# Performance work log

Measured on AMD Instinct MI355X. Metric: run time of the kernel, lower is better.

The kernel has to match this reference:

```python
import jax, jax.numpy as jnp
import numpy as np
import math

BS, N, D_MODEL, H = 8, 1024, 512, 8
D_K = D_MODEL // H


def setup_inputs() -> dict:
    key = jax.random.key(0)
    ks = jax.random.split(key, 12)
    s = 1.0 / math.sqrt(D_MODEL)
    inp = {
        "query": jax.random.normal(ks[0], (BS, N, D_MODEL), jnp.float32),
        "key": jax.random.normal(ks[1], (BS, N, D_MODEL), jnp.float32),
        "value": jax.random.normal(ks[2], (BS, N, D_MODEL), jnp.float32),
        "wc_matrix": jax.random.normal(ks[3], (BS, N, N), jnp.float32),
        "Wq": jax.random.normal(ks[4], (D_MODEL, D_MODEL), jnp.float32) * s,
        "bq": jnp.zeros((D_MODEL,), jnp.float32),
        "Wk": jax.random.normal(ks[5], (D_MODEL, D_MODEL), jnp.float32) * s,
        "bk": jnp.zeros((D_MODEL,), jnp.float32),
        "Wv": jax.random.normal(ks[6], (D_MODEL, D_MODEL), jnp.float32) * s,
        "bv": jnp.zeros((D_MODEL,), jnp.float32),
        "Wo": jax.random.normal(ks[7], (D_MODEL, D_MODEL), jnp.float32) * s,
        "bo": jnp.zeros((D_MODEL,), jnp.float32),
    }
    return inp


def _split_heads(x):
    # (bs, N, d_model) -> (bs, h, N, d_k)
    b, n, _ = x.shape
    return x.reshape(b, n, H, D_K).transpose(0, 2, 1, 3)


def reference(query, key, value, wc_matrix, Wq, bq, Wk, bk, Wv, bv, Wo, bo):
    # Linear projections (torch Linear: x @ W.T + b), split into heads
    q = _split_heads(query @ Wq.T + bq)
    k = _split_heads(key @ Wk.T + bk)
    v = _split_heads(value @ Wv.T + bv)

    # scores: (bs, h, N, N)
    scores = jnp.einsum("bhnd,bhmd->bhnm", q, k) / jnp.sqrt(jnp.float32(D_K))
    # WC modulation: scores * softmax(wc)[:, None] + scores  (softmax_wc=True, residual=True)
    wc_sm = jax.nn.softmax(wc_matrix, axis=-1)[:, None]  # (bs, 1, N, N)
    scores = scores * wc_sm + scores
    p_attn = jax.nn.softmax(scores, axis=-1)  # dropout is identity in eval

    a = jnp.einsum("bhnm,bhmd->bhnd", p_attn, v)
    a = a.transpose(0, 2, 1, 3).reshape(query.shape[0], -1, D_MODEL)
    return a @ Wo.T + bo
```

## Files before the change

### kernel.cpp

```cpp
#include <hip/hip_runtime.h>
#include <math.h>


#define BS 8
#define SEQ 1024
#define DM 512
#define NH 8
#define DK 64
#define ROWS (BS * SEQ)

typedef __bf16 bf16_t;
typedef bf16_t bf16x8 __attribute__((ext_vector_type(8)));
typedef bf16_t bf16x4 __attribute__((ext_vector_type(4)));
typedef float f32x4 __attribute__((ext_vector_type(4)));

__device__ inline f32x4 mfma32(bf16x8 a, bf16x8 b, f32x4 c) {
  return __builtin_amdgcn_mfma_f32_16x16x32_bf16(a, b, c, 0, 0, 0);
}

__device__ inline void gload_lds16(const bf16_t* g, bf16_t* l) {
  __builtin_amdgcn_global_load_lds(
      (const __attribute__((address_space(1))) void*)g,
      (__attribute__((address_space(3))) void*)l, 16, 0, 0);
}

__global__ __launch_bounds__(256) void cvt_kernel(
    const float* q, const float* k, const float* v,
    const float* wq, const float* wk, const float* wv, const float* wo,
    bf16_t* xq, bf16_t* xk, bf16_t* xv,
    bf16_t* wqb, bf16_t* wkb, bf16_t* wvb, bf16_t* wob) {
  const float* srcs[7] = {q, k, v, wq, wk, wv, wo};
  bf16_t* dsts[7] = {xq, xk, xv, wqb, wkb, wvb, wob};
  int b = blockIdx.x;
  int seg, boff;
  if (b < 1536) { seg = b >> 9; boff = b & 511; }
  else { seg = 3 + ((b - 1536) >> 5); boff = (b - 1536) & 31; }
  const float* src = srcs[seg] + (size_t)boff * 8192;
  bf16_t* dst = dsts[seg] + (size_t)boff * 8192;
  int t = threadIdx.x;
#pragma unroll
  for (int f = 0; f < 8; ++f) {
    int idx = (f * 256 + t) * 4;
    float4 x = *(const float4*)(src + idx);
    bf16x4 o;
    o[0] = (bf16_t)x.x; o[1] = (bf16_t)x.y; o[2] = (bf16_t)x.z; o[3] = (bf16_t)x.w;
    *(bf16x4*)(dst + idx) = o;
  }
}

__global__ __launch_bounds__(256) void wc_softmax_kernel(const float* __restrict__ wc,
                                                         bf16_t* __restrict__ G) {
  int row = blockIdx.x;
  const float* x = wc + (size_t)row * SEQ;
  bf16_t* y = G + (size_t)row * SEQ;
  int t = threadIdx.x;
  float4 v = *(const float4*)(x + t * 4);
  float m = fmaxf(fmaxf(v.x, v.y), fmaxf(v.z, v.w));
#pragma unroll
  for (int off = 32; off > 0; off >>= 1) m = fmaxf(m, __shfl_xor(m, off, 64));
  __shared__ float sm[4], ss[4];
  int w = t >> 6;
  if ((t & 63) == 0) sm[w] = m;
  __syncthreads();
  m = fmaxf(fmaxf(sm[0], sm[1]), fmaxf(sm[2], sm[3]));
  float4 e;
  e.x = __expf(v.x - m); e.y = __expf(v.y - m);
  e.z = __expf(v.z - m); e.w = __expf(v.w - m);
  float s = e.x + e.y + e.z + e.w;
#pragma unroll
  for (int off = 32; off > 0; off >>= 1) s += __shfl_xor(s, off, 64);
  if ((t & 63) == 0) ss[w] = s;
  __syncthreads();
  s = ss[0] + ss[1] + ss[2] + ss[3];
  float inv = 1.0f / s;
  const float SC = 0.18033688011112042f;
  bf16x4 g;
  g[0] = (bf16_t)((1.0f + e.x * inv) * SC);
  g[1] = (bf16_t)((1.0f + e.y * inv) * SC);
  g[2] = (bf16_t)((1.0f + e.z * inv) * SC);
  g[3] = (bf16_t)((1.0f + e.w * inv) * SC);
  *(bf16x4*)(y + t * 4) = g;
}

template <int BM, bool OUTF32>
__device__ inline void gemm_core(const bf16_t* X, const bf16_t* W,
                                 const float* bias, void* Cv,
                                 int mblk, int nblk) {
  __shared__ bf16_t As[2][BM * 32];
  __shared__ bf16_t Bs[2][128 * 32];
  int t = threadIdx.x, lane = t & 63, w = t >> 6;
  int quad = lane >> 4, l15 = lane & 15;
  constexpr int MT = BM / 32;
  int m0w = (w & 1) * (BM / 2), n0w = (w >> 1) * 64;
  int mbase = mblk * BM, nbase = nblk * 128;
  int lr = lane >> 2, l4 = lane & 3;
  f32x4 acc[MT][4] = {};

#pragma unroll
  for (int f = 0; f < BM / 64; ++f) {
    int i = f * 4 + w;
    gload_lds16(X + (size_t)(mbase + i * 16 + lr) * DM + l4 * 8, &As[0][i * 512]);
  }
#pragma unroll
  for (int f = 0; f < 2; ++f) {
    int i = f * 4 + w;
    gload_lds16(W + (size_t)(nbase + i * 16 + lr) * DM + l4 * 8, &Bs[0][i * 512]);
  }

  for (int it = 0; it < 16; ++it) {
    __syncthreads();
    int cb = it & 1;
    if (it + 1 < 16) {
      int kb = (it + 1) * 32, nb = (it + 1) & 1;
#pragma unroll
      for (int f = 0; f < BM / 64; ++f) {
        int i = f * 4 + w;
        gload_lds16(X + (size_t)(mbase + i * 16 + lr) * DM + kb + l4 * 8, &As[nb][i * 512]);
      }
#pragma unroll
      for (int f = 0; f < 2; ++f) {
        int i = f * 4 + w;
        gload_lds16(W + (size_t)(nbase + i * 16 + lr) * DM + kb + l4 * 8, &Bs[nb][i * 512]);
      }
    }
    bf16x8 af[MT], bfr[4];
#pragma unroll
    for (int mt = 0; mt < MT; ++mt)
      af[mt] = *(const bf16x8*)&As[cb][(m0w + mt * 16 + l15) * 32 + quad * 8];
#pragma unroll
    for (int nt = 0; nt < 4; ++nt)
      bfr[nt] = *(const bf16x8*)&Bs[cb][(n0w + nt * 16 + l15) * 32 + quad * 8];
#pragma unroll
    for (int mt = 0; mt < MT; ++mt)
#pragma unroll
      for (int nt = 0; nt < 4; ++nt)
        acc[mt][nt] = mfma32(af[mt], bfr[nt], acc[mt][nt]);
  }

#pragma unroll
  for (int nt = 0; nt < 4; ++nt) {
    int col = nbase + n0w + nt * 16 + l15;
    float bc = bias[col];
#pragma unroll
    for (int mt = 0; mt < MT; ++mt)
#pragma unroll
      for (int r = 0; r < 4; ++r) {
        int row = mbase + m0w + mt * 16 + quad * 4 + r;
        float vv = acc[mt][nt][r] + bc;
        if (OUTF32)
          ((float*)Cv)[(size_t)row * DM + col] = vv;
        else
          ((bf16_t*)Cv)[(size_t)row * DM + col] = (bf16_t)vv;
      }
  }
}

__global__ __launch_bounds__(256) void gemm_qkv_kernel(
    const bf16_t* xq, const bf16_t* xk, const bf16_t* xv,
    const bf16_t* wq, const bf16_t* wk, const bf16_t* wv,
    const float* bq, const float* bk, const float* bv,
    bf16_t* cq, bf16_t* ck, bf16_t* cv) {
  const bf16_t* Xarr[3] = {xq, xk, xv};
  const bf16_t* Warr[3] = {wq, wk, wv};
  const float* barr[3] = {bq, bk, bv};
  bf16_t* Carr[3] = {cq, ck, cv};
  int z = blockIdx.z;
  gemm_core<128, false>(Xarr[z], Warr[z], barr[z], Carr[z], blockIdx.x, blockIdx.y);
}

__global__ __launch_bounds__(256) void gemm_wo_kernel(const bf16_t* X, const bf16_t* W,
                                                      const float* bias, float* C) {
  gemm_core<64, true>(X, W, bias, C, blockIdx.x, blockIdx.y);
}

__global__ __launch_bounds__(256) void vtrans_kernel(const bf16_t* __restrict__ Vb,
                                                     bf16_t* __restrict__ Vt) {
  int mt = blockIdx.x;
  int bh = blockIdx.y;
  int b = bh >> 3, h = bh & 7;
  __shared__ bf16_t Ts[64][66];
  int t = threadIdx.x;
#pragma unroll
  for (int f = 0; f < 2; ++f) {
    int chunk = t + f * 256;
    int row = chunk >> 3;
    int c8 = (chunk & 7) * 8;
    bf16x8 v = *(const bf16x8*)&Vb[(size_t)(b * SEQ + mt * 64 + row) * DM + h * DK + c8];
#pragma unroll
    for (int j = 0; j < 8; ++j) Ts[c8 + j][row] = v[j];
  }
  __syncthreads();
#pragma unroll
  for (int f = 0; f < 2; ++f) {
    int chunk = t + f * 256;
    int d = chunk >> 3;
    int m8 = (chunk & 7) * 8;
    bf16x8 o;
#pragma unroll
    for (int j = 0; j < 8; ++j) o[j] = Ts[d][m8 + j];
    *(bf16x8*)&Vt[((size_t)(bh * DK + d)) * SEQ + mt * 64 + m8] = o;
  }
}

__global__ __launch_bounds__(256, 4) void flash_mfma_kernel(
    const bf16_t* __restrict__ Qb, const bf16_t* __restrict__ Kb,
    const bf16_t* __restrict__ Vt, const bf16_t* __restrict__ G,
    bf16_t* __restrict__ Ab) {
  int flat = blockIdx.x + 16 * (blockIdx.y + 8 * blockIdx.z);
  int l = (flat & 7) * 128 + (flat >> 3);
  int qt = l & 15, h = (l >> 4) & 7, b = l >> 7;

  __shared__ bf16_t Ks[2][64 * 64];
  __shared__ bf16_t Vs[2][64 * 64];
  __shared__ bf16_t Ps[4][16 * 64];
  int t = threadIdx.x, lane = t & 63, w = t >> 6;
  int quad = lane >> 4, l15 = lane & 15;
  int k7 = l15 & 7;

  int srow[2], scol[2];
#pragma unroll
  for (int f = 0; f < 2; ++f) {
    int idx = f * 256 + t;
    int r = idx >> 3, p = idx & 7;
    srow[f] = r;
    scol[f] = ((p ^ (r & 7)) * 8);
  }
  const bf16_t* Kbase = Kb + (size_t)(b * SEQ) * DM + h * DK;
  const bf16_t* Vbase = Vt + (size_t)((b * NH + h) * DK) * SEQ;

  size_t qrow_g = (size_t)(b * SEQ + qt * 64 + w * 16 + l15) * DM + h * DK;
  bf16x8 aq0 = *(const bf16x8*)&Qb[qrow_g + quad * 8];
  bf16x8 aq1 = *(const bf16x8*)&Qb[qrow_g + 32 + quad * 8];

  const size_t grow = (size_t)(b * SEQ + qt * 64 + w * 16 + l15) * SEQ;
  bf16x4 greg[4];
#pragma unroll
  for (int ct = 0; ct < 4; ++ct)
    greg[ct] = *(const bf16x4*)&G[grow + ct * 16 + quad * 4];

#pragma unroll
  for (int f = 0; f < 2; ++f) {
    int cbase = (f * 256 + w * 64) * 8;
    gload_lds16(Kbase + (size_t)srow[f] * DM + scol[f], &Ks[0][cbase]);
    gload_lds16(Vbase + (size_t)srow[f] * SEQ + scol[f], &Vs[0][cbase]);
  }
  asm volatile("s_waitcnt vmcnt(0)" ::: "memory");

  float l_st = 0.f;
  f32x4 o[4] = {};

  for (int mt = 0; mt < 16; ++mt) {
    asm volatile("s_barrier" ::: "memory");
    int cb = mt & 1;
    if (mt < 15) {
      int nb = cb ^ 1;
      const bf16_t* Kn = Kbase + (size_t)(mt + 1) * 64 * DM;
      const bf16_t* Vn = Vbase + (mt + 1) * 64;
#pragma unroll
      for (int f = 0; f < 2; ++f) {
        int cbase = (f * 256 + w * 64) * 8;
        gload_lds16(Kn + (size_t)srow[f] * DM + scol[f], &Ks[nb][cbase]);
        gload_lds16(Vn + (size_t)srow[f] * SEQ + scol[f], &Vs[nb][cbase]);
      }
      asm volatile("s_waitcnt vmcnt(8)" ::: "memory");
    } else {
      asm volatile("s_waitcnt vmcnt(4)" ::: "memory");
    }

    f32x4 s[4];
    __builtin_amdgcn_s_setprio(1);
#pragma unroll
    for (int ct = 0; ct < 4; ++ct) {
      int r = ct * 16 + l15;
      int sw = r & 7;
      bf16x8 ak0 = *(const bf16x8*)&Ks[cb][r * 64 + ((quad ^ sw) * 8)];
      bf16x8 ak1 = *(const bf16x8*)&Ks[cb][r * 64 + (((4 + quad) ^ sw) * 8)];
      f32x4 z = {};
      s[ct] = mfma32(ak1, aq1, mfma32(ak0, aq0, z));
    }
    __builtin_amdgcn_s_setprio(0);

    float rs = 0.f;
#pragma unroll
    for (int ct = 0; ct < 4; ++ct) {
      bf16x4 pb;
#pragma unroll
      for (int r = 0; r < 4; ++r) {
        float p = __builtin_amdgcn_exp2f(s[ct][r] * (float)greg[ct][r]);
        pb[r] = (bf16_t)p;
        rs += p;
      }
      int chunk = (2 * ct + (quad >> 1)) ^ k7;
      *(bf16x4*)&Ps[w][l15 * 64 + chunk * 8 + (quad & 1) * 4] = pb;
    }
    if (mt < 15) {
#pragma unroll
      for (int ct = 0; ct < 4; ++ct)
        greg[ct] = *(const bf16x4*)&G[grow + (mt + 1) * 64 + ct * 16 + quad * 4];
    }
    rs += __shfl_xor(rs, 16, 64);
    rs += __shfl_xor(rs, 32, 64);
    l_st += rs;

    __builtin_amdgcn_s_setprio(1);
#pragma unroll
    for (int c = 0; c < 2; ++c) {
      int pchunk = (4 * c + quad) ^ k7;
      bf16x8 bp = *(const bf16x8*)&Ps[w][l15 * 64 + pchunk * 8];
#pragma unroll
      for (int dt = 0; dt < 4; ++dt) {
        int d = dt * 16 + l15;
        int vchunk = (4 * c + quad) ^ (d & 7);
        bf16x8 av = *(const bf16x8*)&Vs[cb][d * 64 + vchunk * 8];
        o[dt] = mfma32(av, bp, o[dt]);
      }
    }
    __builtin_amdgcn_s_setprio(0);
  }

  float linv = 1.0f / l_st;
  size_t orow = (size_t)(b * SEQ + qt * 64 + w * 16 + l15) * DM + h * DK;
#pragma unroll
  for (int dt = 0; dt < 4; ++dt) {
    bf16x4 ov;
#pragma unroll
    for (int r = 0; r < 4; ++r) ov[r] = (bf16_t)(o[dt][r] * linv);
    *(bf16x4*)&Ab[orow + dt * 16 + quad * 4] = ov;
  }
}

extern "C" void kernel_launch(void* const* d_in, const int* in_sizes, int n_in,
                              void* d_out, int out_size, void* d_ws, size_t ws_size,
                              hipStream_t stream) {
  const float* query = (const float*)d_in[0];
  const float* key = (const float*)d_in[1];
  const float* value = (const float*)d_in[2];
  const float* wc = (const float*)d_in[3];
  const float* Wq = (const float*)d_in[4];
  const float* bq = (const float*)d_in[5];
  const float* Wk = (const float*)d_in[6];
  const float* bk = (const float*)d_in[7];
  const float* Wv = (const float*)d_in[8];
  const float* bv = (const float*)d_in[9];
  const float* Wo = (const float*)d_in[10];
  const float* bo = (const float*)d_in[11];
  float* out = (float*)d_out;

  const size_t ACT = (size_t)ROWS * DM;
  const size_t WSZ = (size_t)DM * DM;
  bf16_t* Qb = (bf16_t*)d_ws;
  bf16_t* Kb = Qb + ACT;
  bf16_t* Vb = Kb + ACT;
  bf16_t* Vt = Vb + ACT;
  bf16_t* Ab = Vt + ACT;
  bf16_t* G = Ab + ACT;
  bf16_t* Xq = G + (size_t)BS * SEQ * SEQ;
  bf16_t* Xk = Xq + ACT;
  bf16_t* Xv = Xk + ACT;
  bf16_t* Wqb = Xv + ACT;
  bf16_t* Wkb = Wqb + WSZ;
  bf16_t* Wvb = Wkb + WSZ;
  bf16_t* Wob = Wvb + WSZ;

  cvt_kernel<<<1664, 256, 0, stream>>>(query, key, value, Wq, Wk, Wv, Wo,
                                       Xq, Xk, Xv, Wqb, Wkb, Wvb, Wob);

  wc_softmax_kernel<<<BS * SEQ, 256, 0, stream>>>(wc, G);

  gemm_qkv_kernel<<<dim3(ROWS / 128, DM / 128, 3), 256, 0, stream>>>(
      Xq, Xk, Xv, Wqb, Wkb, Wvb, bq, bk, bv, Qb, Kb, Vb);

  vtrans_kernel<<<dim3(16, 64), 256, 0, stream>>>(Vb, Vt);

  flash_mfma_kernel<<<dim3(SEQ / 64, NH, BS), 256, 0, stream>>>(Qb, Kb, Vt, G, Ab);

  gemm_wo_kernel<<<dim3(ROWS / 64, DM / 128), 256, 0, stream>>>(Ab, Wob, bo, out);
}
```

Measured before the change: 225.1 us.

## Use 32x32x16 MFMA in attention with 128-row query tiles and fuse prep kernels

The attention kernel now uses 32x32x16 bf16 MFMA instructions, with each wave owning 32 query rows. Each block covers 128 queries, so the grid is halved and each K/V tile loaded into LDS serves twice as many queries. The barrier and wait placement is reordered so the wait on the next tile happens after the PV stage, and the per-iteration row-sum shuffle is replaced by a single final shuffle. The conversion and wc-softmax kernels are merged into one launch to save a launch. The risks are higher register pressure from the 16-float accumulators and lower occupancy, since the occupancy hint was removed and there are only 512 blocks.

```diff
diff --git a/kernel.cpp b/kernel.cpp
--- a/kernel.cpp
+++ b/kernel.cpp
@@ -13,9 +13,13 @@
 typedef bf16_t bf16x8 __attribute__((ext_vector_type(8)));
 typedef bf16_t bf16x4 __attribute__((ext_vector_type(4)));
 typedef float f32x4 __attribute__((ext_vector_type(4)));
+typedef float f32x16 __attribute__((ext_vector_type(16)));
 
 __device__ inline f32x4 mfma32(bf16x8 a, bf16x8 b, f32x4 c) {
   return __builtin_amdgcn_mfma_f32_16x16x32_bf16(a, b, c, 0, 0, 0);
+}
+__device__ inline f32x16 mfma3232(bf16x8 a, bf16x8 b, f32x16 c) {
+  return __builtin_amdgcn_mfma_f32_32x32x16_bf16(a, b, c, 0, 0, 0);
 }
 
 __device__ inline void gload_lds16(const bf16_t* g, bf16_t* l) {
@@ -24,62 +28,61 @@
       (__attribute__((address_space(3))) void*)l, 16, 0, 0);
 }
 
-__global__ __launch_bounds__(256) void cvt_kernel(
+__global__ __launch_bounds__(256) void prep_kernel(
     const float* q, const float* k, const float* v,
     const float* wq, const float* wk, const float* wv, const float* wo,
     bf16_t* xq, bf16_t* xk, bf16_t* xv,
-    bf16_t* wqb, bf16_t* wkb, bf16_t* wvb, bf16_t* wob) {
-  const float* srcs[7] = {q, k, v, wq, wk, wv, wo};
-  bf16_t* dsts[7] = {xq, xk, xv, wqb, wkb, wvb, wob};
-  int b = blockIdx.x;
-  int seg, boff;
-  if (b < 1536) { seg = b >> 9; boff = b & 511; }
-  else { seg = 3 + ((b - 1536) >> 5); boff = (b - 1536) & 31; }
-  const float* src = srcs[seg] + (size_t)boff * 8192;
-  bf16_t* dst = dsts[seg] + (size_t)boff * 8192;
+    bf16_t* wqb, bf16_t* wkb, bf16_t* wvb, bf16_t* wob,
+    const float* __restrict__ wc, bf16_t* __restrict__ G) {
+  int bx = blockIdx.x;
   int t = threadIdx.x;
-#pragma unroll
-  for (int f = 0; f < 8; ++f) {
-    int idx = (f * 256 + t) * 4;
-    float4 x = *(const float4*)(src + idx);
-    bf16x4 o;
-    o[0] = (bf16_t)x.x; o[1] = (bf16_t)x.y; o[2] = (bf16_t)x.z; o[3] = (bf16_t)x.w;
-    *(bf16x4*)(dst + idx) = o;
-  }
-}
-
-__global__ __launch_bounds__(256) void wc_softmax_kernel(const float* __restrict__ wc,
-                                                         bf16_t* __restrict__ G) {
-  int row = blockIdx.x;
-  const float* x = wc + (size_t)row * SEQ;
-  bf16_t* y = G + (size_t)row * SEQ;
-  int t = threadIdx.x;
-  float4 v = *(const float4*)(x + t * 4);
-  float m = fmaxf(fmaxf(v.x, v.y), fmaxf(v.z, v.w));
-#pragma unroll
-  for (int off = 32; off > 0; off >>= 1) m = fmaxf(m, __shfl_xor(m, off, 64));
-  __shared__ float sm[4], ss[4];
-  int w = t >> 6;
-  if ((t & 63) == 0) sm[w] = m;
-  __syncthreads();
-  m = fmaxf(fmaxf(sm[0], sm[1]), fmaxf(sm[2], sm[3]));
-  float4 e;
-  e.x = __expf(v.x - m); e.y = __expf(v.y - m);
-  e.z = __expf(v.z - m); e.w = __expf(v.w - m);
-  float s = e.x + e.y + e.z + e.w;
-#pragma unroll
-  for (int off = 32; off > 0; off >>= 1) s += __shfl_xor(s, off, 64);
-  if ((t & 63) == 0) ss[w] = s;
-  __syncthreads();
-  s = ss[0] + ss[1] + ss[2] + ss[3];
-  float inv = 1.0f / s;
-  const float SC = 0.18033688011112042f;
-  bf16x4 g;
-  g[0] = (bf16_t)((1.0f + e.x * inv) * SC);
-  g[1] = (bf16_t)((1.0f + e.y * inv) * SC);
-  g[2] = (bf16_t)((1.0f + e.z * inv) * SC);
-  g[3] = (bf16_t)((1.0f + e.w * inv) * SC);
-  *(bf16x4*)(y + t * 4) = g;
+  if (bx < 1664) {
+    const float* srcs[7] = {q, k, v, wq, wk, wv, wo};
+    bf16_t* dsts[7] = {xq, xk, xv, wqb, wkb, wvb, wob};
+    int seg, boff;
+    if (bx < 1536) { seg = bx >> 9; boff = bx & 511; }
+    else { seg = 3 + ((bx - 1536) >> 5); boff = (bx - 1536) & 31; }
+    const float* src = srcs[seg] + (size_t)boff * 8192;
+    bf16_t* dst = dsts[seg] + (size_t)boff * 8192;
+#pragma unroll
+    for (int f = 0; f < 8; ++f) {
+      int idx = (f * 256 + t) * 4;
+      float4 x = *(const float4*)(src + idx);
+      bf16x4 o;
+      o[0] = (bf16_t)x.x; o[1] = (bf16_t)x.y; o[2] = (bf16_t)x.z; o[3] = (bf16_t)x.w;
+      *(bf16x4*)(dst + idx) = o;
+    }
+  } else {
+    int row = bx - 1664;
+    const float* x = wc + (size_t)row * SEQ;
+    bf16_t* y = G + (size_t)row * SEQ;
+    float4 vv = *(const float4*)(x + t * 4);
+    float m = fmaxf(fmaxf(vv.x, vv.y), fmaxf(vv.z, vv.w));
+#pragma unroll
+    for (int off = 32; off > 0; off >>= 1) m = fmaxf(m, __shfl_xor(m, off, 64));
+    __shared__ float sm[4], ss[4];
+    int w = t >> 6;
+    if ((t & 63) == 0) sm[w] = m;
+    __syncthreads();
+    m = fmaxf(fmaxf(sm[0], sm[1]), fmaxf(sm[2], sm[3]));
+    float4 e;
+    e.x = __expf(vv.x - m); e.y = __expf(vv.y - m);
+    e.z = __expf(vv.z - m); e.w = __expf(vv.w - m);
+    float s = e.x + e.y + e.z + e.w;
+#pragma unroll
+    for (int off = 32; off > 0; off >>= 1) s += __shfl_xor(s, off, 64);
+    if ((t & 63) == 0) ss[w] = s;
+    __syncthreads();
+    s = ss[0] + ss[1] + ss[2] + ss[3];
+    float inv = 1.0f / s;
+    const float SC = 0.18033688011112042f;
+    bf16x4 g;
+    g[0] = (bf16_t)((1.0f + e.x * inv) * SC);
+    g[1] = (bf16_t)((1.0f + e.y * inv) * SC);
+    g[2] = (bf16_t)((1.0f + e.z * inv) * SC);
+    g[3] = (bf16_t)((1.0f + e.w * inv) * SC);
+    *(bf16x4*)(y + t * 4) = g;
+  }
 }
 
 template <int BM, bool OUTF32>
@@ -202,20 +205,21 @@
   }
 }
 
-__global__ __launch_bounds__(256, 4) void flash_mfma_kernel(
+__global__ __launch_bounds__(256) void flash_mfma_kernel(
     const bf16_t* __restrict__ Qb, const bf16_t* __restrict__ Kb,
     const bf16_t* __restrict__ Vt, const bf16_t* __restrict__ G,
     bf16_t* __restrict__ Ab) {
-  int flat = blockIdx.x + 16 * (blockIdx.y + 8 * blockIdx.z);
-  int l = (flat & 7) * 128 + (flat >> 3);
-  int qt = l & 15, h = (l >> 4) & 7, b = l >> 7;
+  int flat = blockIdx.x + 8 * (blockIdx.y + 8 * blockIdx.z);
+  int l = (flat & 7) * 64 + (flat >> 3);
+  int qt = l & 7, h = (l >> 3) & 7, b = l >> 6;
 
   __shared__ bf16_t Ks[2][64 * 64];
   __shared__ bf16_t Vs[2][64 * 64];
-  __shared__ bf16_t Ps[4][16 * 64];
+  __shared__ bf16_t Ps[4][32 * 64];
+
   int t = threadIdx.x, lane = t & 63, w = t >> 6;
-  int quad = lane >> 4, l15 = lane & 15;
-  int k7 = l15 & 7;
+  int l31 = lane & 31, lh = lane >> 5;
+  int s7 = l31 & 7;
 
   int srow[2], scol[2];
 #pragma unroll
@@ -228,15 +232,11 @@
   const bf16_t* Kbase = Kb + (size_t)(b * SEQ) * DM + h * DK;
   const bf16_t* Vbase = Vt + (size_t)((b * NH + h) * DK) * SEQ;
 
-  size_t qrow_g = (size_t)(b * SEQ + qt * 64 + w * 16 + l15) * DM + h * DK;
-  bf16x8 aq0 = *(const bf16x8*)&Qb[qrow_g + quad * 8];
-  bf16x8 aq1 = *(const bf16x8*)&Qb[qrow_g + 32 + quad * 8];
-
-  const size_t grow = (size_t)(b * SEQ + qt * 64 + w * 16 + l15) * SEQ;
-  bf16x4 greg[4];
-#pragma unroll
-  for (int ct = 0; ct < 4; ++ct)
-    greg[ct] = *(const bf16x4*)&G[grow + ct * 16 + quad * 4];
+  size_t qrow_g = (size_t)(b * SEQ + qt * 128 + w * 32 + l31) * DM + h * DK;
+  bf16x8 aq[4];
+#pragma unroll
+  for (int ks = 0; ks < 4; ++ks)
+    aq[ks] = *(const bf16x8*)&Qb[qrow_g + ks * 16 + lh * 8];
 
 #pragma unroll
   for (int f = 0; f < 2; ++f) {
@@ -244,13 +244,23 @@
     gload_lds16(Kbase + (size_t)srow[f] * DM + scol[f], &Ks[0][cbase]);
     gload_lds16(Vbase + (size_t)srow[f] * SEQ + scol[f], &Vs[0][cbase]);
   }
-  asm volatile("s_waitcnt vmcnt(0)" ::: "memory");
+  asm volatile("" ::: "memory");
+
+  const size_t grow = (size_t)(b * SEQ + qt * 128 + w * 32 + l31) * SEQ;
+  bf16x4 greg[8];
+#pragma unroll
+  for (int kt = 0; kt < 2; ++kt)
+#pragma unroll
+    for (int g4 = 0; g4 < 4; ++g4)
+      greg[kt * 4 + g4] = *(const bf16x4*)&G[grow + kt * 32 + g4 * 8 + lh * 4];
+
+  asm volatile("s_waitcnt vmcnt(8)" ::: "memory");
+  asm volatile("s_barrier" ::: "memory");
 
   float l_st = 0.f;
-  f32x4 o[4] = {};
+  f32x16 o0 = {}, o1 = {};
 
   for (int mt = 0; mt < 16; ++mt) {
-    asm volatile("s_barrier" ::: "memory");
     int cb = mt & 1;
     if (mt < 15) {
       int nb = cb ^ 1;
@@ -262,70 +272,80 @@
         gload_lds16(Kn + (size_t)srow[f] * DM + scol[f], &Ks[nb][cbase]);
         gload_lds16(Vn + (size_t)srow[f] * SEQ + scol[f], &Vs[nb][cbase]);
       }
+      asm volatile("" ::: "memory");
+    }
+
+    f32x16 st0 = {}, st1 = {};
+    __builtin_amdgcn_s_setprio(1);
+#pragma unroll
+    for (int ks = 0; ks < 4; ++ks) {
+      int c = ((ks * 2 + lh) ^ s7) * 8;
+      bf16x8 ak0 = *(const bf16x8*)&Ks[cb][l31 * 64 + c];
+      bf16x8 ak1 = *(const bf16x8*)&Ks[cb][(32 + l31) * 64 + c];
+      st0 = mfma3232(ak0, aq[ks], st0);
+      st1 = mfma3232(ak1, aq[ks], st1);
+    }
+    __builtin_amdgcn_s_setprio(0);
+
+    float rs = 0.f;
+    auto dosm = [&](const f32x16& st, int kt) {
+#pragma unroll
+      for (int g4 = 0; g4 < 4; ++g4) {
+        bf16x4 pb;
+#pragma unroll
+        for (int rr = 0; rr < 4; ++rr) {
+          float p = __builtin_amdgcn_exp2f(st[g4 * 4 + rr] *
+                                           (float)greg[kt * 4 + g4][rr]);
+          pb[rr] = (bf16_t)p;
+          rs += p;
+        }
+        *(bf16x4*)&Ps[w][l31 * 64 + (((kt * 4 + g4) ^ s7) * 8) + lh * 4] = pb;
+      }
+    };
+    dosm(st0, 0);
+    dosm(st1, 1);
+    l_st += rs;
+
+    if (mt < 15) {
+#pragma unroll
+      for (int kt = 0; kt < 2; ++kt)
+#pragma unroll
+        for (int g4 = 0; g4 < 4; ++g4)
+          greg[kt * 4 + g4] = *(const bf16x4*)&G[grow + (mt + 1) * 64 +
+                                                 kt * 32 + g4 * 8 + lh * 4];
+    }
+
+    __builtin_amdgcn_s_setprio(1);
+#pragma unroll
+    for (int ks = 0; ks < 4; ++ks) {
+      int c = ((ks * 2 + lh) ^ s7) * 8;
+      bf16x8 bp = *(const bf16x8*)&Ps[w][l31 * 64 + c];
+      bf16x8 av0 = *(const bf16x8*)&Vs[cb][l31 * 64 + c];
+      bf16x8 av1 = *(const bf16x8*)&Vs[cb][(32 + l31) * 64 + c];
+      o0 = mfma3232(av0, bp, o0);
+      o1 = mfma3232(av1, bp, o1);
+    }
+    __builtin_amdgcn_s_setprio(0);
+
+    if (mt < 15) {
       asm volatile("s_waitcnt vmcnt(8)" ::: "memory");
-    } else {
-      asm volatile("s_waitcnt vmcnt(4)" ::: "memory");
-    }
-
-    f32x4 s[4];
-    __builtin_amdgcn_s_setprio(1);
-#pragma unroll
-    for (int ct = 0; ct < 4; ++ct) {
-      int r = ct * 16 + l15;
-      int sw = r & 7;
-      bf16x8 ak0 = *(const bf16x8*)&Ks[cb][r * 64 + ((quad ^ sw) * 8)];
-      bf16x8 ak1 = *(const bf16x8*)&Ks[cb][r * 64 + (((4 + quad) ^ sw) * 8)];
-      f32x4 z = {};
-      s[ct] = mfma32(ak1, aq1, mfma32(ak0, aq0, z));
-    }
-    __builtin_amdgcn_s_setprio(0);
-
-    float rs = 0.f;
-#pragma unroll
-    for (int ct = 0; ct < 4; ++ct) {
-      bf16x4 pb;
-#pragma unroll
-      for (int r = 0; r < 4; ++r) {
-        float p = __builtin_amdgcn_exp2f(s[ct][r] * (float)greg[ct][r]);
-        pb[r] = (bf16_t)p;
-        rs += p;
-      }
-      int chunk = (2 * ct + (quad >> 1)) ^ k7;
-      *(bf16x4*)&Ps[w][l15 * 64 + chunk * 8 + (quad & 1) * 4] = pb;
-    }
-    if (mt < 15) {
-#pragma unroll
-      for (int ct = 0; ct < 4; ++ct)
-        greg[ct] = *(const bf16x4*)&G[grow + (mt + 1) * 64 + ct * 16 + quad * 4];
-    }
-    rs += __shfl_xor(rs, 16, 64);
-    rs += __shfl_xor(rs, 32, 64);
-    l_st += rs;
-
-    __builtin_amdgcn_s_setprio(1);
-#pragma unroll
-    for (int c = 0; c < 2; ++c) {
-      int pchunk = (4 * c + quad) ^ k7;
-      bf16x8 bp = *(const bf16x8*)&Ps[w][l15 * 64 + pchunk * 8];
-#pragma unroll
-      for (int dt = 0; dt < 4; ++dt) {
-        int d = dt * 16 + l15;
-        int vchunk = (4 * c + quad) ^ (d & 7);
-        bf16x8 av = *(const bf16x8*)&Vs[cb][d * 64 + vchunk * 8];
-        o[dt] = mfma32(av, bp, o[dt]);
-      }
-    }
-    __builtin_amdgcn_s_setprio(0);
-  }
-
+      asm volatile("s_barrier" ::: "memory");
+    }
+  }
+
+  l_st += __shfl_xor(l_st, 32, 64);
   float linv = 1.0f / l_st;
-  size_t orow = (size_t)(b * SEQ + qt * 64 + w * 16 + l15) * DM + h * DK;
-#pragma unroll
-  for (int dt = 0; dt < 4; ++dt) {
-    bf16x4 ov;
-#pragma unroll
-    for (int r = 0; r < 4; ++r) ov[r] = (bf16_t)(o[dt][r] * linv);
-    *(bf16x4*)&Ab[orow + dt * 16 + quad * 4] = ov;
+
+#pragma unroll
+  for (int dt = 0; dt < 2; ++dt) {
+    const f32x16& o = dt ? o1 : o0;
+#pragma unroll
+    for (int g4 = 0; g4 < 4; ++g4) {
+      bf16x4 ov;
+#pragma unroll
+      for (int rr = 0; rr < 4; ++rr) ov[rr] = (bf16_t)(o[g4 * 4 + rr] * linv);
+      *(bf16x4*)&Ab[qrow_g + dt * 32 + g4 * 8 + lh * 4] = ov;
+    }
   }
 }
 
@@ -362,17 +382,16 @@
   bf16_t* Wvb = Wkb + WSZ;
   bf16_t* Wob = Wvb + WSZ;
 
-  cvt_kernel<<<1664, 256, 0, stream>>>(query, key, value, Wq, Wk, Wv, Wo,
-                                       Xq, Xk, Xv, Wqb, Wkb, Wvb, Wob);
-
-  wc_softmax_kernel<<<BS * SEQ, 256, 0, stream>>>(wc, G);
+  prep_kernel<<<1664 + BS * SEQ, 256, 0, stream>>>(
+      query, key, value, Wq, Wk, Wv, Wo,
+      Xq, Xk, Xv, Wqb, Wkb, Wvb, Wob, wc, G);
 
   gemm_qkv_kernel<<<dim3(ROWS / 128, DM / 128, 3), 256, 0, stream>>>(
       Xq, Xk, Xv, Wqb, Wkb, Wvb, bq, bk, bv, Qb, Kb, Vb);
 
   vtrans_kernel<<<dim3(16, 64), 256, 0, stream>>>(Vb, Vt);
 
-  flash_mfma_kernel<<<dim3(SEQ / 64, NH, BS), 256, 0, stream>>>(Qb, Kb, Vt, G, Ab);
+  flash_mfma_kernel<<<dim3(SEQ / 128, NH, BS), 256, 0, stream>>>(Qb, Kb, Vt, G, Ab);
 
   gemm_wo_kernel<<<dim3(ROWS / 64, DM / 128), 256, 0, stream>>>(Ab, Wob, bo, out);
 }
```

After: 223.2 us. No clear change (-0.9%).

## Fuse conversion with wc softmax, write V transposed from GEMM, restructure flash barriers

Applied to the files above, without the earlier changes.

Merges the fp32-to-bf16 conversion kernel and the wc softmax kernel into one launch. The V projection GEMM epilogue now writes directly in the transposed (b,h,d,m) layout, so the separate transpose kernel and its round trip through global memory go away. The flash loop moves its wait and barrier to the end of each iteration so the next K/V prefetch overlaps the current compute. The transposed epilogue writes 4-element bf16 chunks with a stride of SEQ, which may coalesce worse than the old row-major stores.

```diff
diff --git a/kernel.cpp b/kernel.cpp
--- a/kernel.cpp
+++ b/kernel.cpp
@@ -24,65 +24,64 @@
       (__attribute__((address_space(3))) void*)l, 16, 0, 0);
 }
 
-__global__ __launch_bounds__(256) void cvt_kernel(
+__global__ __launch_bounds__(256) void prep_kernel(
     const float* q, const float* k, const float* v,
     const float* wq, const float* wk, const float* wv, const float* wo,
     bf16_t* xq, bf16_t* xk, bf16_t* xv,
-    bf16_t* wqb, bf16_t* wkb, bf16_t* wvb, bf16_t* wob) {
-  const float* srcs[7] = {q, k, v, wq, wk, wv, wo};
-  bf16_t* dsts[7] = {xq, xk, xv, wqb, wkb, wvb, wob};
-  int b = blockIdx.x;
-  int seg, boff;
-  if (b < 1536) { seg = b >> 9; boff = b & 511; }
-  else { seg = 3 + ((b - 1536) >> 5); boff = (b - 1536) & 31; }
-  const float* src = srcs[seg] + (size_t)boff * 8192;
-  bf16_t* dst = dsts[seg] + (size_t)boff * 8192;
+    bf16_t* wqb, bf16_t* wkb, bf16_t* wvb, bf16_t* wob,
+    const float* __restrict__ wc, bf16_t* __restrict__ G) {
+  int bx = blockIdx.x;
   int t = threadIdx.x;
-#pragma unroll
-  for (int f = 0; f < 8; ++f) {
-    int idx = (f * 256 + t) * 4;
-    float4 x = *(const float4*)(src + idx);
-    bf16x4 o;
-    o[0] = (bf16_t)x.x; o[1] = (bf16_t)x.y; o[2] = (bf16_t)x.z; o[3] = (bf16_t)x.w;
-    *(bf16x4*)(dst + idx) = o;
-  }
-}
-
-__global__ __launch_bounds__(256) void wc_softmax_kernel(const float* __restrict__ wc,
-                                                         bf16_t* __restrict__ G) {
-  int row = blockIdx.x;
-  const float* x = wc + (size_t)row * SEQ;
-  bf16_t* y = G + (size_t)row * SEQ;
-  int t = threadIdx.x;
-  float4 v = *(const float4*)(x + t * 4);
-  float m = fmaxf(fmaxf(v.x, v.y), fmaxf(v.z, v.w));
-#pragma unroll
-  for (int off = 32; off > 0; off >>= 1) m = fmaxf(m, __shfl_xor(m, off, 64));
-  __shared__ float sm[4], ss[4];
-  int w = t >> 6;
-  if ((t & 63) == 0) sm[w] = m;
-  __syncthreads();
-  m = fmaxf(fmaxf(sm[0], sm[1]), fmaxf(sm[2], sm[3]));
-  float4 e;
-  e.x = __expf(v.x - m); e.y = __expf(v.y - m);
-  e.z = __expf(v.z - m); e.w = __expf(v.w - m);
-  float s = e.x + e.y + e.z + e.w;
-#pragma unroll
-  for (int off = 32; off > 0; off >>= 1) s += __shfl_xor(s, off, 64);
-  if ((t & 63) == 0) ss[w] = s;
-  __syncthreads();
-  s = ss[0] + ss[1] + ss[2] + ss[3];
-  float inv = 1.0f / s;
-  const float SC = 0.18033688011112042f;
-  bf16x4 g;
-  g[0] = (bf16_t)((1.0f + e.x * inv) * SC);
-  g[1] = (bf16_t)((1.0f + e.y * inv) * SC);
-  g[2] = (bf16_t)((1.0f + e.z * inv) * SC);
-  g[3] = (bf16_t)((1.0f + e.w * inv) * SC);
-  *(bf16x4*)(y + t * 4) = g;
-}
-
-template <int BM, bool OUTF32>
+  if (bx < 1664) {
+    const float* srcs[7] = {q, k, v, wq, wk, wv, wo};
+    bf16_t* dsts[7] = {xq, xk, xv, wqb, wkb, wvb, wob};
+    int seg, boff;
+    if (bx < 1536) { seg = bx >> 9; boff = bx & 511; }
+    else { seg = 3 + ((bx - 1536) >> 5); boff = (bx - 1536) & 31; }
+    const float* src = srcs[seg] + (size_t)boff * 8192;
+    bf16_t* dst = dsts[seg] + (size_t)boff * 8192;
+#pragma unroll
+    for (int f = 0; f < 8; ++f) {
+      int idx = (f * 256 + t) * 4;
+      float4 x = *(const float4*)(src + idx);
+      bf16x4 o;
+      o[0] = (bf16_t)x.x; o[1] = (bf16_t)x.y; o[2] = (bf16_t)x.z; o[3] = (bf16_t)x.w;
+      *(bf16x4*)(dst + idx) = o;
+    }
+  } else {
+    int row = bx - 1664;
+    const float* x = wc + (size_t)row * SEQ;
+    bf16_t* y = G + (size_t)row * SEQ;
+    float4 vv = *(const float4*)(x + t * 4);
+    float m = fmaxf(fmaxf(vv.x, vv.y), fmaxf(vv.z, vv.w));
+#pragma unroll
+    for (int off = 32; off > 0; off >>= 1) m = fmaxf(m, __shfl_xor(m, off, 64));
+    __shared__ float sm[4], ss[4];
+    int w = t >> 6;
+    if ((t & 63) == 0) sm[w] = m;
+    __syncthreads();
+    m = fmaxf(fmaxf(sm[0], sm[1]), fmaxf(sm[2], sm[3]));
+    float4 e;
+    e.x = __expf(vv.x - m); e.y = __expf(vv.y - m);
+    e.z = __expf(vv.z - m); e.w = __expf(vv.w - m);
+    float s = e.x + e.y + e.z + e.w;
+#pragma unroll
+    for (int off = 32; off > 0; off >>= 1) s += __shfl_xor(s, off, 64);
+    if ((t & 63) == 0) ss[w] = s;
+    __syncthreads();
+    s = ss[0] + ss[1] + ss[2] + ss[3];
+    float inv = 1.0f / s;
+    const float SC = 0.18033688011112042f;
+    bf16x4 g;
+    g[0] = (bf16_t)((1.0f + e.x * inv) * SC);
+    g[1] = (bf16_t)((1.0f + e.y * inv) * SC);
+    g[2] = (bf16_t)((1.0f + e.z * inv) * SC);
+    g[3] = (bf16_t)((1.0f + e.w * inv) * SC);
+    *(bf16x4*)(y + t * 4) = g;
+  }
+}
+
+template <int BM, bool OUTF32, bool VTRANS>
 __device__ inline void gemm_core(const bf16_t* X, const bf16_t* W,
                                  const float* bias, void* Cv,
                                  int mblk, int nblk) {
@@ -142,16 +141,27 @@
     int col = nbase + n0w + nt * 16 + l15;
     float bc = bias[col];
 #pragma unroll
-    for (int mt = 0; mt < MT; ++mt)
-#pragma unroll
-      for (int r = 0; r < 4; ++r) {
-        int row = mbase + m0w + mt * 16 + quad * 4 + r;
-        float vv = acc[mt][nt][r] + bc;
-        if (OUTF32)
-          ((float*)Cv)[(size_t)row * DM + col] = vv;
-        else
-          ((bf16_t*)Cv)[(size_t)row * DM + col] = (bf16_t)vv;
-      }
+    for (int mt = 0; mt < MT; ++mt) {
+      if (VTRANS) {
+        int row0 = mbase + m0w + mt * 16 + quad * 4;
+        int b = row0 >> 10, m = row0 & 1023;
+        int h = col >> 6, d = col & 63;
+        bf16x4 ov;
+#pragma unroll
+        for (int r = 0; r < 4; ++r) ov[r] = (bf16_t)(acc[mt][nt][r] + bc);
+        *(bf16x4*)&((bf16_t*)Cv)[((size_t)((b * NH + h) * DK + d)) * SEQ + m] = ov;
+      } else {
+#pragma unroll
+        for (int r = 0; r < 4; ++r) {
+          int row = mbase + m0w + mt * 16 + quad * 4 + r;
+          float vv = acc[mt][nt][r] + bc;
+          if (OUTF32)
+            ((float*)Cv)[(size_t)row * DM + col] = vv;
+          else
+            ((bf16_t*)Cv)[(size_t)row * DM + col] = (bf16_t)vv;
+        }
+      }
+    }
   }
 }
 
@@ -159,47 +169,19 @@
     const bf16_t* xq, const bf16_t* xk, const bf16_t* xv,
     const bf16_t* wq, const bf16_t* wk, const bf16_t* wv,
     const float* bq, const float* bk, const float* bv,
-    bf16_t* cq, bf16_t* ck, bf16_t* cv) {
-  const bf16_t* Xarr[3] = {xq, xk, xv};
-  const bf16_t* Warr[3] = {wq, wk, wv};
-  const float* barr[3] = {bq, bk, bv};
-  bf16_t* Carr[3] = {cq, ck, cv};
+    bf16_t* cq, bf16_t* ck, bf16_t* vt) {
   int z = blockIdx.z;
-  gemm_core<128, false>(Xarr[z], Warr[z], barr[z], Carr[z], blockIdx.x, blockIdx.y);
+  if (z == 0)
+    gemm_core<128, false, false>(xq, wq, bq, cq, blockIdx.x, blockIdx.y);
+  else if (z == 1)
+    gemm_core<128, false, false>(xk, wk, bk, ck, blockIdx.x, blockIdx.y);
+  else
+    gemm_core<128, false, true>(xv, wv, bv, vt, blockIdx.x, blockIdx.y);
 }
 
 __global__ __launch_bounds__(256) void gemm_wo_kernel(const bf16_t* X, const bf16_t* W,
                                                       const float* bias, float* C) {
-  gemm_core<64, true>(X, W, bias, C, blockIdx.x, blockIdx.y);
-}
-
-__global__ __launch_bounds__(256) void vtrans_kernel(const bf16_t* __restrict__ Vb,
-                                                     bf16_t* __restrict__ Vt) {
-  int mt = blockIdx.x;
-  int bh = blockIdx.y;
-  int b = bh >> 3, h = bh & 7;
-  __shared__ bf16_t Ts[64][66];
-  int t = threadIdx.x;
-#pragma unroll
-  for (int f = 0; f < 2; ++f) {
-    int chunk = t + f * 256;
-    int row = chunk >> 3;
-    int c8 = (chunk & 7) * 8;
-    bf16x8 v = *(const bf16x8*)&Vb[(size_t)(b * SEQ + mt * 64 + row) * DM + h * DK + c8];
-#pragma unroll
-    for (int j = 0; j < 8; ++j) Ts[c8 + j][row] = v[j];
-  }
-  __syncthreads();
-#pragma unroll
-  for (int f = 0; f < 2; ++f) {
-    int chunk = t + f * 256;
-    int d = chunk >> 3;
-    int m8 = (chunk & 7) * 8;
-    bf16x8 o;
-#pragma unroll
-    for (int j = 0; j < 8; ++j) o[j] = Ts[d][m8 + j];
-    *(bf16x8*)&Vt[((size_t)(bh * DK + d)) * SEQ + mt * 64 + m8] = o;
-  }
+  gemm_core<64, true, false>(X, W, bias, C, blockIdx.x, blockIdx.y);
 }
 
 __global__ __launch_bounds__(256, 4) void flash_mfma_kernel(
@@ -245,12 +227,12 @@
     gload_lds16(Vbase + (size_t)srow[f] * SEQ + scol[f], &Vs[0][cbase]);
   }
   asm volatile("s_waitcnt vmcnt(0)" ::: "memory");
+  asm volatile("s_barrier" ::: "memory");
 
   float l_st = 0.f;
   f32x4 o[4] = {};
 
   for (int mt = 0; mt < 16; ++mt) {
-    asm volatile("s_barrier" ::: "memory");
     int cb = mt & 1;
     if (mt < 15) {
       int nb = cb ^ 1;
@@ -262,9 +244,7 @@
         gload_lds16(Kn + (size_t)srow[f] * DM + scol[f], &Ks[nb][cbase]);
         gload_lds16(Vn + (size_t)srow[f] * SEQ + scol[f], &Vs[nb][cbase]);
       }
-      asm volatile("s_waitcnt vmcnt(8)" ::: "memory");
-    } else {
-      asm volatile("s_waitcnt vmcnt(4)" ::: "memory");
+      asm volatile("" ::: "memory");
     }
 
     f32x4 s[4];
@@ -316,16 +296,20 @@
       }
     }
     __builtin_amdgcn_s_setprio(0);
+
+    if (mt < 15) {
+      asm volatile("s_waitcnt vmcnt(4)" ::: "memory");
+      asm volatile("s_barrier" ::: "memory");
+    }
   }
 
   float linv = 1.0f / l_st;
-  size_t orow = (size_t)(b * SEQ + qt * 64 + w * 16 + l15) * DM + h * DK;
 #pragma unroll
   for (int dt = 0; dt < 4; ++dt) {
     bf16x4 ov;
 #pragma unroll
     for (int r = 0; r < 4; ++r) ov[r] = (bf16_t)(o[dt][r] * linv);
-    *(bf16x4*)&Ab[orow + dt * 16 + quad * 4] = ov;
+    *(bf16x4*)&Ab[qrow_g + dt * 16 + quad * 4] = ov;
   }
 }
 
@@ -362,15 +346,12 @@
   bf16_t* Wvb = Wkb + WSZ;
   bf16_t* Wob = Wvb + WSZ;
 
-  cvt_kernel<<<1664, 256, 0, stream>>>(query, key, value, Wq, Wk, Wv, Wo,
-                                       Xq, Xk, Xv, Wqb, Wkb, Wvb, Wob);
-
-  wc_softmax_kernel<<<BS * SEQ, 256, 0, stream>>>(wc, G);
+  prep_kernel<<<1664 + BS * SEQ, 256, 0, stream>>>(
+      query, key, value, Wq, Wk, Wv, Wo,
+      Xq, Xk, Xv, Wqb, Wkb, Wvb, Wob, wc, G);
 
   gemm_qkv_kernel<<<dim3(ROWS / 128, DM / 128, 3), 256, 0, stream>>>(
-      Xq, Xk, Xv, Wqb, Wkb, Wvb, bq, bk, bv, Qb, Kb, Vb);
-
-  vtrans_kernel<<<dim3(16, 64), 256, 0, stream>>>(Vb, Vt);
+      Xq, Xk, Xv, Wqb, Wkb, Wvb, bq, bk, bv, Qb, Kb, Vt);
 
   flash_mfma_kernel<<<dim3(SEQ / 64, NH, BS), 256, 0, stream>>>(Qb, Kb, Vt, G, Ab);
 
```

New measurement: 218.4 us. -3.0%, faster.
